# Optimization experiments

Measured on AMD Instinct MI355X. Metric: run time of the kernel, lower is better.

The kernel has to match this reference:

```python
import jax, jax.numpy as jnp
import numpy as np
import math

D_MODEL = 512
HEADS = 8
SHIFT = 1
B, T = 2, 1024


def _layernorm(x, w, b, eps=1e-5):
    mu = jnp.mean(x, -1, keepdims=True)
    var = jnp.mean((x - mu) ** 2, -1, keepdims=True)
    return (x - mu) / jnp.sqrt(var + eps) * w + b


def _l1_cdist(x, w, chunk):
    # x: [N, Din], w: [M, Din] -> [N, M]; chunk over M to bound the broadcast buffer
    N, Din = x.shape
    M = w.shape[0]
    wc = w.reshape(M // chunk, chunk, Din)
    f = lambda wb: jnp.abs(x[:, None, :] - wb[None, :, :]).sum(-1)  # [N, chunk]
    out = jax.lax.map(f, wc)  # [M//chunk, N, chunk]
    return jnp.moveaxis(out, 0, 1).reshape(N, M)


def _proxy_linear(x, w, gain, chunk):
    # ProxyDeltaLinearV68: out = (0.5 - dist_proxy_mean) * gain, dist uses detach trick
    Bx, Tx, Din = x.shape
    xa = jnp.tanh(x).reshape(-1, Din)
    wa = jnp.tanh(w)
    l1 = _l1_cdist(xa, wa, chunk)
    # squared L2 via GEMM (== cdist(p=2)**2), clamped at 0 like torch.cdist
    l2 = jnp.maximum((xa * xa).sum(-1)[:, None] + (wa * wa).sum(-1)[None, :] - 2.0 * (xa @ wa.T), 0.0)
    l1m = l1 / Din
    l2m = l2 / Din
    d = jax.lax.stop_gradient(l1m - l2m) + l2m
    return ((0.5 - d) * gain[None, :]).reshape(Bx, Tx, -1)


def _attention(x, wq_w, wq_g, wk_w, wk_g, wv_w, wv_g, wo_w, wo_b, gamma, rho):
    Bx, Tx, C = x.shape
    H, Dh = HEADS, C // HEADS

    def heads(t):
        return t.reshape(Bx, Tx, H, Dh).transpose(0, 2, 1, 3).reshape(Bx * H, Tx, Dh)

    q = heads(jnp.tanh(_proxy_linear(x, wq_w, wq_g, 32)))
    k = heads(jnp.tanh(_proxy_linear(x, wk_w, wk_g, 32)))
    v = heads(_proxy_linear(x, wv_w, wv_g, 32))
    # pairwise L1 distances, chunked over query positions
    TC = 64
    qr = jnp.moveaxis(q.reshape(Bx * H, Tx // TC, TC, Dh), 1, 0)  # [Tx//TC, BH, TC, Dh]
    f = lambda qb: jnp.abs(qb[:, :, None, :] - k[:, None, :, :]).sum(-1)  # [BH, TC, Tx]
    l1 = jnp.moveaxis(jax.lax.map(f, qr), 0, 1).reshape(Bx * H, Tx, Tx)
    l2 = jnp.maximum((q * q).sum(-1)[:, :, None] + (k * k).sum(-1)[:, None, :]
                     - 2.0 * jnp.einsum('btd,bsd->bts', q, k), 0.0)
    dist = jax.lax.stop_gradient((l1 - l2) / Dh) + l2 / Dh
    dist = dist.reshape(Bx, H, Tx, Tx) * math.sqrt(Dh)
    dsq = dist * dist
    gp = jax.nn.softplus(gamma)[None, :, None, None]
    rp = jax.nn.softplus(rho)[None, :, None, None]
    aw = (1.0 / (1.0 + gp * dsq + 1e-6)) ** rp  # student-t style kernel
    mask = jnp.tril(jnp.ones((Tx, Tx), dtype=bool))
    aw = jnp.where(mask[None, None], aw, 0.0)
    probs = aw / (aw.sum(-1, keepdims=True) + 1e-6)
    out = jnp.einsum('bhts,bhsd->bhtd', probs, v.reshape(Bx, H, Tx, Dh))
    out = out.transpose(0, 2, 1, 3).reshape(Bx, Tx, C)
    return out @ wo_w.T + wo_b


def setup_inputs() -> dict:
    key = jax.random.key(0)
    ks = jax.random.split(key, 10)
    D, Hd = D_MODEL, D_MODEL * 4
    f32 = jnp.float32
    return {
        'x': jax.random.normal(ks[0], (B, T, D), f32),
        'ln1_w': jnp.ones((D,), f32), 'ln1_b': jnp.zeros((D,), f32),
        'wq_w': jax.random.normal(ks[1], (D, D), f32) * 0.1, 'wq_g': jnp.full((D,), 2.0, f32),
        'wk_w': jax.random.normal(ks[2], (D, D), f32) * 0.1, 'wk_g': jnp.full((D,), 2.0, f32),
        'wv_w': jax.random.normal(ks[3], (D, D), f32) * 0.1, 'wv_g': jnp.full((D,), 2.0, f32),
        'wo_w': jax.random.normal(ks[4], (D, D), f32) * 0.02, 'wo_b': jnp.zeros((D,), f32),
        'gamma': jnp.ones((HEADS,), f32), 'rho': jnp.full((HEADS,), 2.0, f32),
        'ln2_w': jnp.ones((D,), f32), 'ln2_b': jnp.zeros((D,), f32),
        'gate_w': jax.random.normal(ks[5], (Hd, D), f32) * 0.1, 'gate_g': jnp.full((Hd,), 2.0, f32),
        'val_w': jax.random.normal(ks[6], (Hd, D), f32) * 0.1, 'val_g': jnp.full((Hd,), 2.0, f32),
        'out_w': jax.random.normal(ks[7], (D, Hd), f32) * 0.1, 'out_g': jnp.full((D,), 2.0, f32),
        'dir_w': jax.random.normal(ks[8], (D,), f32) * 0.1,
    }


def reference(x, ln1_w, ln1_b, wq_w, wq_g, wk_w, wk_g, wv_w, wv_g, wo_w, wo_b,
              gamma, rho, ln2_w, ln2_b, gate_w, gate_g, val_w, val_g, out_w, out_g, dir_w):
    a = _attention(_layernorm(x, ln1_w, ln1_b), wq_w, wq_g, wk_w, wk_g, wv_w, wv_g,
                   wo_w, wo_b, gamma, rho)
    x = x + a  # ATTN_SCALE = 1.0
    h = _layernorm(x, ln2_w, ln2_b)
    gate = jax.nn.silu(_proxy_linear(h, gate_w, gate_g, 32))
    val = _proxy_linear(h, val_w, val_g, 32)
    f = _proxy_linear(gate * val, out_w, out_g, 8)
    # Direction: causal shift of ln2 output, |x_shift - sigmoid(w)|
    xp = jnp.concatenate([jnp.zeros((x.shape[0], SHIFT, x.shape[2]), x.dtype), h[:, :-SHIFT]], axis=1)
    d = jnp.abs(xp - jax.nn.sigmoid(dir_w)[None, None, :])
    return x + f + 0.5 * d  # Delta_SCALE=1.0, DIR_SCALE=0.5, dropout identity (eval)
```

## Files before the change

### kernel.cpp

```cpp
#include <hip/hip_runtime.h>
#include <math.h>


#define NROWS  2048
#define DMODEL 512
#define TSEQ   1024
#define HIDDEN 2048

typedef _Float16 hf;
typedef hf h2 __attribute__((ext_vector_type(2)));
typedef hf h4 __attribute__((ext_vector_type(4)));
typedef hf h8 __attribute__((ext_vector_type(8)));
typedef float f32x4 __attribute__((ext_vector_type(4)));

#if defined(__has_builtin)
#if __has_builtin(__builtin_amdgcn_sad_u8)
#define HAVE_SAD 1
#endif
#if __has_builtin(__builtin_amdgcn_mfma_f32_16x16x32_f16)
#define HAVE_MFMA 1
#endif
#endif

__device__ __forceinline__ unsigned sad8(unsigned a, unsigned b, unsigned c) {
#ifdef HAVE_SAD
  return __builtin_amdgcn_sad_u8(a, b, c);
#else
  unsigned r;
  asm("v_sad_u8 %0, %1, %2, %3" : "=v"(r) : "v"(a), "v"(b), "v"(c));
  return r;
#endif
}

__device__ __forceinline__ float ftanh(float x) {
  const float t = __expf(-2.0f * fabsf(x));
  const float r = (1.0f - t) / (1.0f + t);
  return copysignf(r, x);
}

__device__ __forceinline__ float fpow_ge1(float x, float p) {
  float lg, r;
  asm("v_log_f32 %0, %1" : "=v"(lg) : "v"(x));
  const float e = lg * p;
  asm("v_exp_f32 %0, %1" : "=v"(r) : "v"(e));
  return r;
}

__device__ __forceinline__ unsigned q8(float x) {
  return (unsigned)(int)((x + 1.0f) * 127.5f + 0.5f);
}

struct CP { const float* g0; const float* g1; const float* g2; };

__global__ __launch_bounds__(256) void ln_kernel(
    const float* __restrict__ X, const float* __restrict__ w,
    const float* __restrict__ bb, float* __restrict__ outPlain,
    unsigned char* __restrict__ out8, float4* __restrict__ zf)
{
  const int n = blockIdx.x, tid = threadIdx.x;
  if (zf && tid < 130)
    zf[(size_t)n * 130 + tid] = make_float4(0.f, 0.f, 0.f, 0.f);
  const float* row = X + (size_t)n * DMODEL;
  float2 v = *(const float2*)&row[tid * 2];
  float s1 = v.x + v.y;
  float s2 = v.x * v.x + v.y * v.y;
#pragma unroll
  for (int off = 1; off < 64; off <<= 1) {
    s1 += __shfl_xor(s1, off);
    s2 += __shfl_xor(s2, off);
  }
  __shared__ float red[8];
  if ((tid & 63) == 0) { red[(tid >> 6) * 2] = s1; red[(tid >> 6) * 2 + 1] = s2; }
  __syncthreads();
  s1 = red[0] + red[2] + red[4] + red[6];
  s2 = red[1] + red[3] + red[5] + red[7];
  const float mu   = s1 * (1.0f / DMODEL);
  const float var  = s2 * (1.0f / DMODEL) - mu * mu;
  const float rstd = rsqrtf(var + 1e-5f);
  const int d = tid * 2;
  const float y0 = (v.x - mu) * rstd * w[d]     + bb[d];
  const float y1 = (v.y - mu) * rstd * w[d + 1] + bb[d + 1];
  if (outPlain) *(float2*)&outPlain[(size_t)n * DMODEL + d] = make_float2(y0, y1);
  const unsigned a = q8(ftanh(y0)), b = q8(ftanh(y1));
  *(unsigned short*)&out8[(size_t)n * DMODEL + d] = (unsigned short)(a | (b << 8));
}

__global__ __launch_bounds__(256) void tanhcvt8m_kernel(
    const float* __restrict__ s0, const float* __restrict__ s1,
    const float* __restrict__ s2, unsigned char* __restrict__ out, int K)
{
  const int z = blockIdx.y;
  const float* sb = (z == 0) ? s0 : (z == 1) ? s1 : s2;
  const int rows = (int)gridDim.x * 2;
  const int row = blockIdx.x * 2 + (threadIdx.x >> 7);
  const int t = threadIdx.x & 127;
  const float* src = sb + (size_t)row * K;
  unsigned char* dst = out + ((size_t)z * rows + row) * K;
  for (int k = t * 4; k < K; k += 512) {
    float4 v = *(const float4*)&src[k];
    unsigned pk = q8(ftanh(v.x)) | (q8(ftanh(v.y)) << 8) |
                  (q8(ftanh(v.z)) << 16) | (q8(ftanh(v.w)) << 24);
    *(unsigned*)&dst[k] = pk;
  }
}

template <int NCD, int EPI>
__global__ __launch_bounds__(256, 8) void cdistq_kernel(
    const unsigned char* __restrict__ X8, const unsigned char* __restrict__ W8,
    CP cp,
    unsigned char* __restrict__ o8a, unsigned char* __restrict__ o8b,
    hf* __restrict__ vt16, unsigned char* __restrict__ gvt8,
    unsigned short* __restrict__ pf,
    int M, int K, int Kc, float invK127)
{
  const int m0 = blockIdx.x * 32, n0 = blockIdx.y * 64;
  const int zc = (EPI == 1) ? blockIdx.z : 0;
  const int kb = (EPI == 3) ? blockIdx.z * Kc : 0;
  constexpr int WROW = NCD * 68 + 4;
  __shared__ __align__(16) unsigned xs[2][8][68];
  __shared__ __align__(16) unsigned ws[2][4][WROW];
  const int tid = threadIdx.x, tx = tid & 15, ty = tid >> 4;
  unsigned acc[NCD][4][2] = {};

  const int rs = tid >> 2, ps = (tid & 3) * 2;
  const int half = tid & 127;
  const int wc = (NCD == 2) ? (tid >> 7) : 0;
  const int wcol = half >> 2, pw = (half & 3) * 2;

  const unsigned char* xp = X8 + (size_t)(n0 + rs) * K + kb + (tid & 3) * 8;
  const unsigned char* wq = W8 + (size_t)(zc + wc) * M * K +
                            (size_t)(m0 + wcol) * K + kb + (half & 3) * 8;

  uint2 xv = *(const uint2*)xp;
  uint2 wv = *(const uint2*)wq;

  int p = 0;
#pragma unroll 1
  for (int k0 = 0; k0 < Kc; k0 += 32) {
    xs[p][ps + 0][rs] = xv.x;
    xs[p][ps + 1][rs] = xv.y;
    *(uint2*)&ws[p][pw >> 1][wc * 68 + wcol * 2] = make_uint2(wv.x, wv.y);
    const int kn = (k0 + 32 < Kc) ? k0 + 32 : 0;
    xv = *(const uint2*)(xp + kn);
    wv = *(const uint2*)(wq + kn);
    __syncthreads();

#pragma unroll
    for (int kkp = 0; kkp < 4; kkp++) {
      uint4 a0 = *(const uint4*)&xs[p][kkp * 2 + 0][ty * 4];
      uint4 a1 = *(const uint4*)&xs[p][kkp * 2 + 1][ty * 4];
      const unsigned ae[4] = {a0.x, a0.y, a0.z, a0.w};
      const unsigned ao[4] = {a1.x, a1.y, a1.z, a1.w};
#pragma unroll
      for (int c = 0; c < NCD; c++) {
        uint4 b4 = *(const uint4*)&ws[p][kkp][c * 68 + tx * 4];
#pragma unroll
        for (int i = 0; i < 4; i++) {
          acc[c][i][0] = sad8(ae[i], b4.x, acc[c][i][0]);
          acc[c][i][0] = sad8(ao[i], b4.y, acc[c][i][0]);
          acc[c][i][1] = sad8(ae[i], b4.z, acc[c][i][1]);
          acc[c][i][1] = sad8(ao[i], b4.w, acc[c][i][1]);
        }
      }
    }
    p ^= 1;
  }

  if constexpr (EPI == 1) {
    if (zc < 2) {
      unsigned char* o8 = zc ? o8b : o8a;
      const float* gn = zc ? cp.g1 : cp.g0;
#pragma unroll
      for (int i = 0; i < 4; i++) {
        const int n = n0 + ty * 4 + i;
        unsigned pk = 0;
#pragma unroll
        for (int j = 0; j < 2; j++) {
          const int m = m0 + tx * 2 + j;
          const float val = (0.5f - (float)acc[0][i][j] * invK127) * gn[m];
          pk |= q8(ftanh(val)) << (8 * j);
        }
        *(unsigned short*)&o8[(size_t)n * M + m0 + tx * 2] = (unsigned short)pk;
      }
    } else {
#pragma unroll
      for (int i = 0; i < 4; i++) {
        const int n = n0 + ty * 4 + i;
        const int b = n >> 10, t = n & 1023;
#pragma unroll
        for (int j = 0; j < 2; j++) {
          const int m = m0 + tx * 2 + j;
          const float vv = (0.5f - (float)acc[0][i][j] * invK127) * cp.g2[m];
          vt16[((size_t)(b * 8 + (m >> 6)) * 64 + (m & 63)) * 1024 + t] = (hf)vv;
        }
      }
    }
  } else if constexpr (EPI == 2) {
#pragma unroll
    for (int i = 0; i < 4; i++) {
      const int n = n0 + ty * 4 + i;
      unsigned pk = 0;
#pragma unroll
      for (int j = 0; j < 2; j++) {
        const int m = m0 + tx * 2 + j;
        float g = (0.5f - (float)acc[0][i][j] * invK127) * cp.g0[m];
        g = g / (1.0f + __expf(-g));
        const float vv = (0.5f - (float)acc[1][i][j] * invK127) * cp.g1[m];
        pk |= q8(ftanh(g * vv)) << (8 * j);
      }
      *(unsigned short*)&gvt8[(size_t)n * M + m0 + tx * 2] = (unsigned short)pk;
    }
  } else {
    unsigned short* pz = pf + (size_t)blockIdx.z * ((size_t)NROWS * M);
#pragma unroll
    for (int i = 0; i < 4; i++) {
      const int n = n0 + ty * 4 + i;
      const unsigned p0 = (acc[0][i][0] + 1) >> 1;
      const unsigned p1 = (acc[0][i][1] + 1) >> 1;
      *(unsigned*)&pz[(size_t)n * M + m0 + tx * 2] = p0 | (p1 << 16);
    }
  }
}

__global__ __launch_bounds__(256) void attn_part_kernel(
    const unsigned char* __restrict__ Qb, const unsigned char* __restrict__ Kb,
    const hf* __restrict__ Vt,
    const float* __restrict__ gamma, const float* __restrict__ rho,
    float* __restrict__ accO, float* __restrict__ accR)
{
  const int bh = blockIdx.y, b = bh >> 3, h = bh & 7;
  int rem = 143 - (int)blockIdx.x;
  int tt = 0;
  for (;;) {
    const int nc = ((tt >> 1) + 2) >> 1;
    if (rem < nc) break;
    rem -= nc; ++tt;
  }
  const int ntile = (tt >> 1) + 1;
  const int sb = rem * 2;
  const int se = (sb + 2 < ntile) ? sb + 2 : ntile;
  const int t0 = tt * 32;

  const float gp = log1pf(expf(gamma[h]));
  const float nrp = -log1pf(expf(rho[h]));
  const size_t base8 = ((size_t)b * TSEQ) * DMODEL + h * 64;

  __shared__ unsigned qs8[16][36];
  __shared__ unsigned ks8[16][68];
  __shared__ hf awt[32][72];
  __shared__ hf vsm[64][72];

  const int tid = threadIdx.x, tx = tid & 15, ty = tid >> 4;
  const int tx4 = tx * 4, ty2 = ty * 2;
  const int lane = tid & 63, wv = tid >> 6;
  const float SCALE_D = 1.0f / (127.5f * 8.0f);

  {
    const int r = tid >> 3, p = (tid & 7) * 2;
    uint2 a = *(const uint2*)&Qb[base8 + (size_t)(t0 + r) * DMODEL + (tid & 7) * 8];
    qs8[p + 0][r] = a.x;
    qs8[p + 1][r] = a.y;
  }

  float rsum[2] = {};
  f32x4 cacc[2] = {};

  const int vd = tid >> 2, vs16 = (tid & 3) * 16;
  const int arow = lane & 15;
  const int koff = (lane >> 4) * 8;

  for (int st = sb; st < se; ++st) {
    const int s0 = st * 64;
    __syncthreads();
    {
      const int r = tid >> 2, p = (tid & 3) * 4;
      uint4 a = *(const uint4*)&Kb[base8 + (size_t)(s0 + r) * DMODEL + (tid & 3) * 16];
      ks8[p + 0][r] = a.x;
      ks8[p + 1][r] = a.y;
      ks8[p + 2][r] = a.z;
      ks8[p + 3][r] = a.w;
      const hf* vsrc = &Vt[((size_t)bh * 64 + vd) * 1024 + s0 + vs16];
      *(h8*)&vsm[vd][vs16 + 0] = *(const h8*)vsrc;
      *(h8*)&vsm[vd][vs16 + 8] = *(const h8*)(vsrc + 8);
    }
    __syncthreads();

    unsigned sacc[2][4] = {};
#pragma unroll
    for (int kk = 0; kk < 16; kk++) {
      uint2 qa = *(const uint2*)&qs8[kk][ty2];
      uint4 kb4 = *(const uint4*)&ks8[kk][tx4];
      const unsigned kk4[4] = {kb4.x, kb4.y, kb4.z, kb4.w};
#pragma unroll
      for (int j = 0; j < 4; j++) {
        sacc[0][j] = sad8(qa.x, kk4[j], sacc[0][j]);
        sacc[1][j] = sad8(qa.y, kk4[j], sacc[1][j]);
      }
    }

#pragma unroll
    for (int i = 0; i < 2; i++) {
      const int tg = t0 + ty2 + i;
      h4 pk;
#pragma unroll
      for (int j = 0; j < 4; j++) {
        const int sg = s0 + tx4 + j;
        const float dist = (float)sacc[i][j] * SCALE_D;
        const float bsx = fmaf(gp, dist * dist, 1.0f + 1e-6f);
        float aw = fpow_ge1(bsx, nrp);
        aw = (sg <= tg) ? aw : 0.0f;
        pk[j] = (hf)aw;
        rsum[i] += aw;
      }
      *(h4*)&awt[ty2 + i][tx4] = pk;
    }
    __syncthreads();

#ifdef HAVE_MFMA
#pragma unroll
    for (int ks = 0; ks < 2; ks++) {
      h8 bfrag = *(const h8*)&vsm[wv * 16 + arow][ks * 32 + koff];
      h8 afr0  = *(const h8*)&awt[arow]          [ks * 32 + koff];
      h8 afr1  = *(const h8*)&awt[16 + arow]     [ks * 32 + koff];
      cacc[0] = __builtin_amdgcn_mfma_f32_16x16x32_f16(afr0, bfrag, cacc[0], 0, 0, 0);
      cacc[1] = __builtin_amdgcn_mfma_f32_16x16x32_f16(afr1, bfrag, cacc[1], 0, 0, 0);
    }
#else
    {
      const int crow = (lane >> 4) * 4;
      const int d = wv * 16 + (lane & 15);
#pragma unroll
      for (int mt = 0; mt < 2; mt++)
#pragma unroll
        for (int r = 0; r < 4; r++) {
          const int t = mt * 16 + crow + r;
          float s = cacc[mt][r];
          for (int si = 0; si < 64; si++)
            s += (float)awt[t][si] * (float)vsm[d][si];
          cacc[mt][r] = s;
        }
    }
#endif
  }

#pragma unroll
  for (int off = 1; off < 16; off <<= 1) {
    rsum[0] += __shfl_xor(rsum[0], off);
    rsum[1] += __shfl_xor(rsum[1], off);
  }
  float* aO = accO + ((size_t)bh * TSEQ + t0) * 64;
  {
    const int crow = (lane >> 4) * 4;
    const int ccol = wv * 16 + (lane & 15);
#pragma unroll
    for (int mt = 0; mt < 2; mt++)
#pragma unroll
      for (int r = 0; r < 4; r++)
        atomicAdd(&aO[(size_t)(mt * 16 + crow + r) * 64 + ccol], cacc[mt][r]);
  }
#pragma unroll
  for (int i = 0; i < 2; i++)
    if (tx == 0) atomicAdd(&accR[bh * TSEQ + t0 + ty2 + i], rsum[i]);
}

__global__ __launch_bounds__(256) void gemm_res_kernel(
    const float* __restrict__ Xn, const float* __restrict__ accR,
    const float* __restrict__ W,
    const float* __restrict__ bias, const float* __restrict__ Res,
    float* __restrict__ Out)
{
  const int m0 = blockIdx.x * 64, n0 = blockIdx.y * 64;
  __shared__ float xs[16][68];
  __shared__ float wsm[16][68];
  const int tid = threadIdx.x, tx = tid & 15, ty = tid >> 4;
  const int lr = tid >> 2, lc4 = (tid & 3) * 4;
  float acc[4][4] = {};
  const int n = n0 + lr;
  const float* wp = &W[(size_t)(m0 + lr) * DMODEL + lc4];
  for (int k0 = 0; k0 < DMODEL; k0 += 16) {
    const int c = k0 + lc4;
    const size_t arow = ((size_t)((n >> 10) * 8 + (c >> 6))) * TSEQ + (n & 1023);
    float4 xv = *(const float4*)&Xn[arow * 64 + (c & 63)];
    const float inv = 1.0f / (accR[arow] + 1e-6f);
    xv.x *= inv; xv.y *= inv; xv.z *= inv; xv.w *= inv;
    float4 wv = *(const float4*)(wp + k0);
    __syncthreads();
    xs [lc4 + 0][lr] = xv.x; xs [lc4 + 1][lr] = xv.y; xs [lc4 + 2][lr] = xv.z; xs [lc4 + 3][lr] = xv.w;
    wsm[lc4 + 0][lr] = wv.x; wsm[lc4 + 1][lr] = wv.y; wsm[lc4 + 2][lr] = wv.z; wsm[lc4 + 3][lr] = wv.w;
    __syncthreads();
#pragma unroll
    for (int kk = 0; kk < 16; kk++) {
      float4 av = *(const float4*)&xs[kk][ty * 4];
      float4 bv = *(const float4*)&wsm[kk][tx * 4];
      const float aa[4] = {av.x, av.y, av.z, av.w};
      const float bs[4] = {bv.x, bv.y, bv.z, bv.w};
#pragma unroll
      for (int i = 0; i < 4; i++)
#pragma unroll
        for (int j = 0; j < 4; j++) acc[i][j] = fmaf(aa[i], bs[j], acc[i][j]);
    }
  }
#pragma unroll
  for (int i = 0; i < 4; i++) {
    const int nn = n0 + ty * 4 + i;
    float o[4];
#pragma unroll
    for (int j = 0; j < 4; j++) {
      const int m = m0 + tx * 4 + j;
      o[j] = acc[i][j] + bias[m] + Res[(size_t)nn * DMODEL + m];
    }
    *(float4*)&Out[(size_t)nn * DMODEL + m0 + tx * 4] = make_float4(o[0], o[1], o[2], o[3]);
  }
}

__global__ void final_kernel(const float* __restrict__ x2,
                             const unsigned short* __restrict__ pf,
                             const float* __restrict__ outg,
                             const float* __restrict__ h,
                             const float* __restrict__ dirw,
                             float* __restrict__ out)
{
  const int i4 = blockIdx.x * 256 + threadIdx.x;
  const int n = i4 >> 7;
  const int t = n & (TSEQ - 1);
  const int d4 = (i4 & 127) * 4;
  float4 xv = *(const float4*)&x2[(size_t)i4 * 4];
  const size_t off = (size_t)i4 * 4;
  unsigned s[4] = {};
#pragma unroll
  for (int z = 0; z < 4; z++) {
    uint2 a = *(const uint2*)&pf[(size_t)z * ((size_t)NROWS * DMODEL) + off];
    s[0] += (a.x & 0xffffu);
    s[1] += (a.x >> 16);
    s[2] += (a.y & 0xffffu);
    s[3] += (a.y >> 16);
  }
  float4 hv = make_float4(0.f, 0.f, 0.f, 0.f);
  if (t != 0) hv = *(const float4*)&h[(size_t)(i4 - 128) * 4];
  const float xx[4] = {xv.x, xv.y, xv.z, xv.w};
  const float hh[4] = {hv.x, hv.y, hv.z, hv.w};
  const float invf = 2.0f / (127.5f * 2048.0f);
  float o[4];
#pragma unroll
  for (int j = 0; j < 4; j++) {
    const float f = (0.5f - (float)s[j] * invf) * outg[d4 + j];
    const float sg = 1.0f / (1.0f + __expf(-dirw[d4 + j]));
    o[j] = xx[j] + f + 0.5f * fabsf(hh[j] - sg);
  }
  *(float4*)&out[(size_t)i4 * 4] = make_float4(o[0], o[1], o[2], o[3]);
}

extern "C" void kernel_launch(void* const* d_in, const int* in_sizes, int n_in,
                              void* d_out, int out_size, void* d_ws, size_t ws_size,
                              hipStream_t stream)
{
  (void)in_sizes; (void)n_in; (void)out_size;
  const float* x      = (const float*)d_in[0];
  const float* ln1_w  = (const float*)d_in[1];
  const float* ln1_b  = (const float*)d_in[2];
  const float* wq_w   = (const float*)d_in[3];
  const float* wq_g   = (const float*)d_in[4];
  const float* wk_w   = (const float*)d_in[5];
  const float* wk_g   = (const float*)d_in[6];
  const float* wv_w   = (const float*)d_in[7];
  const float* wv_g   = (const float*)d_in[8];
  const float* wo_w   = (const float*)d_in[9];
  const float* wo_b   = (const float*)d_in[10];
  const float* gamma  = (const float*)d_in[11];
  const float* rho    = (const float*)d_in[12];
  const float* ln2_w  = (const float*)d_in[13];
  const float* ln2_b  = (const float*)d_in[14];
  const float* gate_w = (const float*)d_in[15];
  const float* gate_g = (const float*)d_in[16];
  const float* val_w  = (const float*)d_in[17];
  const float* val_g  = (const float*)d_in[18];
  const float* out_w  = (const float*)d_in[19];
  const float* out_g  = (const float*)d_in[20];
  const float* dir_w  = (const float*)d_in[21];
  float* out = (float*)d_out;

  if (ws_size < ((size_t)32 << 20)) return;
  unsigned char* wsb = (unsigned char*)d_ws;

  unsigned char* w8   = wsb;
  unsigned char* x8   = wsb + ((size_t)2 << 20);
  unsigned char* q8b  = wsb + ((size_t)3 << 20);
  unsigned char* k8b  = wsb + ((size_t)4 << 20);
  hf*            vt16 = (hf*)(wsb + ((size_t)5 << 20));
  unsigned char* gvt8 = wsb + ((size_t)7 << 20);
  float*         accO = (float*)(wsb + ((size_t)11 << 20));
  float*         accR = (float*)(wsb + ((size_t)15 << 20));
  unsigned short* pf  = (unsigned short*)(wsb + ((size_t)16 << 20));
  float*         x2   = (float*)(wsb + ((size_t)24 << 20));
  float*         hbuf = (float*)(wsb + ((size_t)28 << 20));

  ln_kernel<<<NROWS, 256, 0, stream>>>(x, ln1_w, ln1_b, nullptr, x8,
                                       (float4*)accO);

  tanhcvt8m_kernel<<<dim3(256, 3), 256, 0, stream>>>(wq_w, wk_w, wv_w, w8, 512);

  {
    CP cp; cp.g0 = wq_g; cp.g1 = wk_g; cp.g2 = wv_g;
    cdistq_kernel<1, 1><<<dim3(16, 32, 3), 256, 0, stream>>>(
        x8, w8, cp, q8b, k8b, vt16, nullptr, nullptr,
        512, 512, 512, 1.0f / (127.5f * 512.0f));
  }

  attn_part_kernel<<<dim3(144, 16), 256, 0, stream>>>(q8b, k8b, vt16,
                                                      gamma, rho, accO, accR);

  gemm_res_kernel<<<dim3(8, 32), 256, 0, stream>>>(accO, accR, wo_w, wo_b, x, x2);

  ln_kernel<<<NROWS, 256, 0, stream>>>(x2, ln2_w, ln2_b, hbuf, x8, nullptr);

  tanhcvt8m_kernel<<<dim3(1024, 2), 256, 0, stream>>>(gate_w, val_w, val_w, w8, 512);

  {
    CP cp; cp.g0 = gate_g; cp.g1 = val_g; cp.g2 = nullptr;
    cdistq_kernel<2, 2><<<dim3(64, 32, 1), 256, 0, stream>>>(
        x8, w8, cp, nullptr, nullptr, nullptr, gvt8, nullptr,
        2048, 512, 512, 1.0f / (127.5f * 512.0f));
  }

  tanhcvt8m_kernel<<<dim3(256, 1), 256, 0, stream>>>(out_w, out_w, out_w, w8, 2048);

  {
    CP cp; cp.g0 = out_g; cp.g1 = nullptr; cp.g2 = nullptr;
    cdistq_kernel<1, 3><<<dim3(16, 32, 4), 256, 0, stream>>>(
        gvt8, w8, cp, nullptr, nullptr, nullptr, nullptr, pf,
        512, 2048, 512, 0.0f);
  }

  final_kernel<<<1024, 256, 0, stream>>>(x2, pf, out_g, hbuf, dir_w, out);
}
```

Measured before the change: 160.1 us.

## Fuse layernorm with weight quantization launches and double cdist K-step

New measurement: 150.8 us. 1.06x faster.

```diff
diff --git a/kernel.cpp b/kernel.cpp
--- a/kernel.cpp
+++ b/kernel.cpp
@@ -52,12 +52,12 @@
 
 struct CP { const float* g0; const float* g1; const float* g2; };
 
-__global__ __launch_bounds__(256) void ln_kernel(
-    const float* __restrict__ X, const float* __restrict__ w,
+__device__ __forceinline__ void ln_body(
+    int n, const float* __restrict__ X, const float* __restrict__ w,
     const float* __restrict__ bb, float* __restrict__ outPlain,
     unsigned char* __restrict__ out8, float4* __restrict__ zf)
 {
-  const int n = blockIdx.x, tid = threadIdx.x;
+  const int tid = threadIdx.x;
   if (zf && tid < 130)
     zf[(size_t)n * 130 + tid] = make_float4(0.f, 0.f, 0.f, 0.f);
   const float* row = X + (size_t)n * DMODEL;
@@ -85,22 +85,54 @@
   *(unsigned short*)&out8[(size_t)n * DMODEL + d] = (unsigned short)(a | (b << 8));
 }
 
-__global__ __launch_bounds__(256) void tanhcvt8m_kernel(
-    const float* __restrict__ s0, const float* __restrict__ s1,
-    const float* __restrict__ s2, unsigned char* __restrict__ out, int K)
-{
-  const int z = blockIdx.y;
-  const float* sb = (z == 0) ? s0 : (z == 1) ? s1 : s2;
-  const int rows = (int)gridDim.x * 2;
-  const int row = blockIdx.x * 2 + (threadIdx.x >> 7);
+__device__ __forceinline__ void cvt_body(
+    const float* __restrict__ src, unsigned char* __restrict__ dst, int K)
+{
   const int t = threadIdx.x & 127;
-  const float* src = sb + (size_t)row * K;
-  unsigned char* dst = out + ((size_t)z * rows + row) * K;
   for (int k = t * 4; k < K; k += 512) {
     float4 v = *(const float4*)&src[k];
     unsigned pk = q8(ftanh(v.x)) | (q8(ftanh(v.y)) << 8) |
                   (q8(ftanh(v.z)) << 16) | (q8(ftanh(v.w)) << 24);
     *(unsigned*)&dst[k] = pk;
+  }
+}
+
+__global__ __launch_bounds__(256) void fused1_kernel(
+    const float* __restrict__ X, const float* __restrict__ lw,
+    const float* __restrict__ lb, unsigned char* __restrict__ x8,
+    float4* __restrict__ zf,
+    const float* __restrict__ wq, const float* __restrict__ wk,
+    const float* __restrict__ wv, unsigned char* __restrict__ w8)
+{
+  const int b = blockIdx.x;
+  if (b < NROWS) { ln_body(b, X, lw, lb, nullptr, x8, zf); return; }
+  const int c = b - NROWS;
+  const int z = c >> 8, rb = c & 255;
+  const float* sb = (z == 0) ? wq : (z == 1) ? wk : wv;
+  const int row = rb * 2 + (threadIdx.x >> 7);
+  cvt_body(sb + (size_t)row * 512, w8 + ((size_t)z * 512 + row) * 512, 512);
+}
+
+__global__ __launch_bounds__(256) void fused6_kernel(
+    const float* __restrict__ x2, const float* __restrict__ lw,
+    const float* __restrict__ lb, float* __restrict__ hbuf,
+    unsigned char* __restrict__ x8,
+    const float* __restrict__ gate_w, const float* __restrict__ val_w,
+    unsigned char* __restrict__ w8,
+    const float* __restrict__ out_w, unsigned char* __restrict__ w9)
+{
+  const int b = blockIdx.x;
+  if (b < NROWS) { ln_body(b, x2, lw, lb, hbuf, x8, nullptr); return; }
+  int c = b - NROWS;
+  if (c < 2048) {
+    const int z = c >> 10, rb = c & 1023;
+    const float* sb = z ? val_w : gate_w;
+    const int row = rb * 2 + (threadIdx.x >> 7);
+    cvt_body(sb + (size_t)row * 512, w8 + ((size_t)z * 2048 + row) * 512, 512);
+  } else {
+    c -= 2048;
+    const int row = c * 2 + (threadIdx.x >> 7);
+    cvt_body(out_w + (size_t)row * 2048, w9 + (size_t)row * 2048, 2048);
   }
 }
 
@@ -117,36 +149,43 @@
   const int zc = (EPI == 1) ? blockIdx.z : 0;
   const int kb = (EPI == 3) ? blockIdx.z * Kc : 0;
   constexpr int WROW = NCD * 68 + 4;
-  __shared__ __align__(16) unsigned xs[2][8][68];
-  __shared__ __align__(16) unsigned ws[2][4][WROW];
+  __shared__ __align__(16) unsigned xs[2][16][68];
+  __shared__ __align__(16) unsigned ws[2][8][WROW];
   const int tid = threadIdx.x, tx = tid & 15, ty = tid >> 4;
   unsigned acc[NCD][4][2] = {};
 
   const int rs = tid >> 2, ps = (tid & 3) * 2;
   const int half = tid & 127;
   const int wc = (NCD == 2) ? (tid >> 7) : 0;
-  const int wcol = half >> 2, pw = (half & 3) * 2;
+  const int wcol = half >> 2, kkw = half & 3;
 
   const unsigned char* xp = X8 + (size_t)(n0 + rs) * K + kb + (tid & 3) * 8;
   const unsigned char* wq = W8 + (size_t)(zc + wc) * M * K +
-                            (size_t)(m0 + wcol) * K + kb + (half & 3) * 8;
-
-  uint2 xv = *(const uint2*)xp;
-  uint2 wv = *(const uint2*)wq;
+                            (size_t)(m0 + wcol) * K + kb + kkw * 8;
+
+  uint2 xv0 = *(const uint2*)xp;
+  uint2 xv1 = *(const uint2*)(xp + 32);
+  uint2 wv0 = *(const uint2*)wq;
+  uint2 wv1 = *(const uint2*)(wq + 32);
 
   int p = 0;
 #pragma unroll 1
-  for (int k0 = 0; k0 < Kc; k0 += 32) {
-    xs[p][ps + 0][rs] = xv.x;
-    xs[p][ps + 1][rs] = xv.y;
-    *(uint2*)&ws[p][pw >> 1][wc * 68 + wcol * 2] = make_uint2(wv.x, wv.y);
-    const int kn = (k0 + 32 < Kc) ? k0 + 32 : 0;
-    xv = *(const uint2*)(xp + kn);
-    wv = *(const uint2*)(wq + kn);
+  for (int k0 = 0; k0 < Kc; k0 += 64) {
+    xs[p][ps + 0][rs] = xv0.x;
+    xs[p][ps + 1][rs] = xv0.y;
+    xs[p][8 + ps + 0][rs] = xv1.x;
+    xs[p][8 + ps + 1][rs] = xv1.y;
+    *(uint2*)&ws[p][kkw][wc * 68 + wcol * 2]     = make_uint2(wv0.x, wv0.y);
+    *(uint2*)&ws[p][4 + kkw][wc * 68 + wcol * 2] = make_uint2(wv1.x, wv1.y);
+    const int kn = (k0 + 64 < Kc) ? k0 + 64 : 0;
+    xv0 = *(const uint2*)(xp + kn);
+    xv1 = *(const uint2*)(xp + kn + 32);
+    wv0 = *(const uint2*)(wq + kn);
+    wv1 = *(const uint2*)(wq + kn + 32);
     __syncthreads();
 
 #pragma unroll
-    for (int kkp = 0; kkp < 4; kkp++) {
+    for (int kkp = 0; kkp < 8; kkp++) {
       uint4 a0 = *(const uint4*)&xs[p][kkp * 2 + 0][ty * 4];
       uint4 a1 = *(const uint4*)&xs[p][kkp * 2 + 1][ty * 4];
       const unsigned ae[4] = {a0.x, a0.y, a0.z, a0.w};
@@ -487,6 +526,7 @@
   unsigned char* q8b  = wsb + ((size_t)3 << 20);
   unsigned char* k8b  = wsb + ((size_t)4 << 20);
   hf*            vt16 = (hf*)(wsb + ((size_t)5 << 20));
+  unsigned char* w9   = wsb + ((size_t)5 << 20);
   unsigned char* gvt8 = wsb + ((size_t)7 << 20);
   float*         accO = (float*)(wsb + ((size_t)11 << 20));
   float*         accR = (float*)(wsb + ((size_t)15 << 20));
@@ -494,10 +534,8 @@
   float*         x2   = (float*)(wsb + ((size_t)24 << 20));
   float*         hbuf = (float*)(wsb + ((size_t)28 << 20));
 
-  ln_kernel<<<NROWS, 256, 0, stream>>>(x, ln1_w, ln1_b, nullptr, x8,
-                                       (float4*)accO);
-
-  tanhcvt8m_kernel<<<dim3(256, 3), 256, 0, stream>>>(wq_w, wk_w, wv_w, w8, 512);
+  fused1_kernel<<<NROWS + 768, 256, 0, stream>>>(
+      x, ln1_w, ln1_b, x8, (float4*)accO, wq_w, wk_w, wv_w, w8);
 
   {
     CP cp; cp.g0 = wq_g; cp.g1 = wk_g; cp.g2 = wv_g;
@@ -511,9 +549,8 @@
 
   gemm_res_kernel<<<dim3(8, 32), 256, 0, stream>>>(accO, accR, wo_w, wo_b, x, x2);
 
-  ln_kernel<<<NROWS, 256, 0, stream>>>(x2, ln2_w, ln2_b, hbuf, x8, nullptr);
-
-  tanhcvt8m_kernel<<<dim3(1024, 2), 256, 0, stream>>>(gate_w, val_w, val_w, w8, 512);
+  fused6_kernel<<<NROWS + 2048 + 256, 256, 0, stream>>>(
+      x2, ln2_w, ln2_b, hbuf, x8, gate_w, val_w, w8, out_w, w9);
 
   {
     CP cp; cp.g0 = gate_g; cp.g1 = val_g; cp.g2 = nullptr;
@@ -522,12 +559,10 @@
         2048, 512, 512, 1.0f / (127.5f * 512.0f));
   }
 
-  tanhcvt8m_kernel<<<dim3(256, 1), 256, 0, stream>>>(out_w, out_w, out_w, w8, 2048);
-
   {
     CP cp; cp.g0 = out_g; cp.g1 = nullptr; cp.g2 = nullptr;
     cdistq_kernel<1, 3><<<dim3(16, 32, 4), 256, 0, stream>>>(
-        gvt8, w8, cp, nullptr, nullptr, nullptr, nullptr, pf,
+        gvt8, w9, cp, nullptr, nullptr, nullptr, nullptr, pf,
         512, 2048, 512, 0.0f);
   }
 
```
